# Kernel tuning notes

Measured on AMD Instinct MI355X. Metric: run time of the kernel, lower is better.

The kernel has to match this reference:

```python
import jax, jax.numpy as jnp
import numpy as np
from jax import lax

B, BERT_DIM, Z_DIM, ODE_UNITS, T_MAX = 4096, 768, 64, 128, 512
LN_EPS = 1e-5

def _glorot(key, shape):
    fan_in, fan_out = shape[0], shape[1]
    lim = float(np.sqrt(6.0 / (fan_in + fan_out)))
    return jax.random.uniform(key, shape, jnp.float32, -lim, lim)

def setup_inputs() -> dict:
    key = jax.random.key(0)
    ks = jax.random.split(key, 16)
    inp = {
        'bert_emb': jax.random.normal(ks[0], (B, BERT_DIM), jnp.float32),
        'times': jax.random.uniform(ks[1], (B, T_MAX), jnp.float32),
        'seq_lens': jax.random.randint(ks[2], (B,), 0, T_MAX).astype(jnp.int64),
        'eps': jax.random.normal(ks[3], (B, Z_DIM), jnp.float32),
        # bert_proj: Linear(768->64) + LayerNorm(64)
        'proj_W': _glorot(ks[4], (BERT_DIM, Z_DIM)),
        'proj_b': jnp.zeros((Z_DIM,), jnp.float32),
        'ln_g': jnp.ones((Z_DIM,), jnp.float32),
        'ln_b': jnp.zeros((Z_DIM,), jnp.float32),
        # DiffusionAug
        'log_noise_std': jnp.float32(-2.0),
        'den_W1': _glorot(ks[5], (Z_DIM, 2 * Z_DIM)),
        'den_b1': jnp.zeros((2 * Z_DIM,), jnp.float32),
        'den_W2': _glorot(ks[6], (2 * Z_DIM, Z_DIM)),
        'den_b2': jnp.zeros((Z_DIM,), jnp.float32),
        # ODEFunc: Linear->Tanh->Linear->Tanh->Linear (xavier_uniform, zero bias)
        'ode_W1': _glorot(ks[7], (Z_DIM, ODE_UNITS)),
        'ode_b1': jnp.zeros((ODE_UNITS,), jnp.float32),
        'ode_W2': _glorot(ks[8], (ODE_UNITS, ODE_UNITS)),
        'ode_b2': jnp.zeros((ODE_UNITS,), jnp.float32),
        'ode_W3': _glorot(ks[9], (ODE_UNITS, Z_DIM)),
        'ode_b3': jnp.zeros((Z_DIM,), jnp.float32),
        # dec_head: Linear(64->2)
        'dec_W': _glorot(ks[10], (Z_DIM, 2)),
        'dec_b': jnp.zeros((2,), jnp.float32),
    }
    return inp

def reference(bert_emb, times, seq_lens, eps, proj_W, proj_b, ln_g, ln_b,
              log_noise_std, den_W1, den_b1, den_W2, den_b2,
              ode_W1, ode_b1, ode_W2, ode_b2, ode_W3, ode_b3, dec_W, dec_b):
    T = times.shape[1]
    # bert_proj: Linear + LayerNorm (dropout = identity in eval)
    h = bert_emb @ proj_W + proj_b
    mu = jnp.mean(h, axis=-1, keepdims=True)
    var = jnp.var(h, axis=-1, keepdims=True)
    z_clean = (h - mu) * lax.rsqrt(var + LN_EPS) * ln_g + ln_b
    # DiffusionAug: noise + denoise MLP, MSE to detached clean latent
    sigma = jax.nn.softplus(log_noise_std)
    z_noisy = z_clean + sigma * eps
    z_aug = jax.nn.silu(z_noisy @ den_W1 + den_b1) @ den_W2 + den_b2
    diff_loss = jnp.mean((z_aug - lax.stop_gradient(z_clean)) ** 2)
    # Euler ODE integration: z <- z + dt * f(z), T sequential steps
    dt = jnp.float32(1.0 / max(T, 1))
    def step(z, _):
        f = jnp.tanh(jnp.tanh(z @ ode_W1 + ode_b1) @ ode_W2 + ode_b2) @ ode_W3 + ode_b3
        z_new = z + dt * f
        return z_new, z_new
    _, zs = lax.scan(step, z_aug, None, length=T)  # zs: (T, B, z)
    traj = jnp.concatenate([z_aug[:, None, :], jnp.swapaxes(zs, 0, 1)], axis=1)  # (B, T+1, z)
    out = traj @ dec_W + dec_b  # (B, T+1, 2)
    pred_delta = out[:, :, 0]
    stop_logits = out[:, :, 1]
    return (pred_delta, stop_logits, diff_loss)
```

## Files before the change

### kernel.cpp

```cpp
#include <hip/hip_runtime.h>
#include <stdint.h>

#define NB 4096
#define NT 512
#define OT 513
#define TOTE (NB*OT)
#define LOSSOFF (2*TOTE)

typedef float  f32x4 __attribute__((ext_vector_type(4)));
typedef __fp16 f16x8 __attribute__((ext_vector_type(8)));
typedef __fp16 f16x2 __attribute__((ext_vector_type(2)));

#define MFMA(A,B,C) __builtin_amdgcn_mfma_f32_16x16x32_f16((A),(B),(C),0,0,0)

__device__ __forceinline__ void wg_barrier() {
  asm volatile("s_waitcnt lgkmcnt(0)\n\ts_barrier" ::: "memory");
}

__device__ __forceinline__ float fast_tanh(float x) {
  float e = __builtin_amdgcn_exp2f(x * 2.8853900817779268f);
  return __builtin_fmaf(-2.0f, __builtin_amdgcn_rcpf(1.0f + e), 1.0f);
}
__device__ __forceinline__ float fast_silu(float x) {
  float e = __builtin_amdgcn_exp2f(x * -1.4426950408889634f);
  return x * __builtin_amdgcn_rcpf(1.0f + e);
}
__device__ __forceinline__ uint32_t pk2(float a, float b) {
  union { f16x2 h; uint32_t u; } c;
  c.h = __builtin_amdgcn_cvt_pkrtz(a, b);
  return c.u;
}
__device__ __forceinline__ f16x8 pack8(f32x4 a, f32x4 b) {
  union { f16x8 v; f16x2 h[4]; } u;
  u.h[0] = __builtin_amdgcn_cvt_pkrtz(a.x, a.y);
  u.h[1] = __builtin_amdgcn_cvt_pkrtz(a.z, a.w);
  u.h[2] = __builtin_amdgcn_cvt_pkrtz(b.x, b.y);
  u.h[3] = __builtin_amdgcn_cvt_pkrtz(b.z, b.w);
  return u.v;
}

#define WS_CBUF (256u<<10)

__global__ void prep_kernel(const float* __restrict__ oW1, const float* __restrict__ oW2,
                            const float* __restrict__ dW,  const float* __restrict__ dW1,
                            const float* __restrict__ dW2, const float* __restrict__ pW,
                            const float* __restrict__ oW3, const float* __restrict__ ob3,
                            char* __restrict__ wdst, float* __restrict__ cbuf,
                            float* __restrict__ dout) {
  const float dtc = 1.0f / 512.0f;
  if (blockIdx.x == 57) {
    int tid = threadIdx.x;
    if (tid < 144) {
      float s = 0.f;
      if (tid < 128) {
        for (int k = 0; k < 64; k++) s = __builtin_fmaf(ob3[k], oW1[k * 128 + tid], s);
      } else if (tid < 130) {
        int cc = tid - 128;
        for (int k = 0; k < 64; k++) s = __builtin_fmaf(ob3[k], dW[k * 2 + cc], s);
      }
      cbuf[tid] = s * dtc;
    }
    if (tid == 255) dout[LOSSOFF] = 0.0f;
    return;
  }
  int g = blockIdx.x * 256 + threadIdx.x;
  int fid = g >> 6, lane = g & 63;
  if (fid >= 50 && fid < 64) return;
  int m4 = lane & 15;
  int k0 = (lane >> 4) * 8;
  if (fid >= 48 && fid < 50) {
    int kt = fid - 48;
    int kb = kt * 32 + k0;
    f16x8 out;
    #pragma unroll
    for (int j = 0; j < 8; j++) out[j] = (m4 < 2) ? (__fp16)dW[(kb + j) * 2 + m4] : (__fp16)0.f;
    *(f16x8*)(wdst + (size_t)(fid * 64 + lane) * 16) = out;
    return;
  }
  if (fid >= 192) {
    int local = fid - 192;
    int mt = local >> 2, kt = local & 3;
    int m  = mt * 16 + m4;
    int kb = kt * 32 + k0;
    f16x8 out;
    #pragma unroll
    for (int j = 0; j < 8; j++) {
      int k = kb + j;
      float s = 0.f;
      if (m < 128) {
        #pragma unroll 4
        for (int i = 0; i < 64; i++) s = __builtin_fmaf(oW3[k * 64 + i], oW1[i * 128 + m], s);
      } else if (m < 130) {
        for (int i = 0; i < 64; i++) s = __builtin_fmaf(oW3[k * 64 + i], dW[i * 2 + (m - 128)], s);
      }
      out[j] = (__fp16)(s * dtc);
    }
    *(f16x8*)(wdst + (size_t)(fid * 64 + lane) * 16) = out;
    return;
  }
  const float* src; int Kt, M, base;
  if      (fid < 16)  { src = oW1;  Kt = 2;  M = 128; base = 0;  }
  else if (fid < 48)  { src = oW2;  Kt = 4;  M = 128; base = 16; }
  else if (fid < 80)  { src = dW1;  Kt = 2;  M = 128; base = 64; }
  else if (fid < 96)  { src = dW2;  Kt = 4;  M = 64;  base = 80; }
  else                { src = pW;   Kt = 24; M = 64;  base = 96; }
  int local = fid - base;
  int mt = local / Kt, kt = local % Kt;
  int m  = mt * 16 + m4;
  int kb = kt * 32 + k0;
  f16x8 out;
  #pragma unroll
  for (int j = 0; j < 8; j++) out[j] = (__fp16)src[(size_t)(kb + j) * M + m];
  *(f16x8*)(wdst + (size_t)(fid * 64 + lane) * 16) = out;
}

__global__ __launch_bounds__(512, 1) void main_kernel(
    const float* __restrict__ bert, const float* __restrict__ eps,
    const float* __restrict__ projb, const float* __restrict__ lng,
    const float* __restrict__ lnb,  const float* __restrict__ lns,
    const float* __restrict__ db1,  const float* __restrict__ db2,
    const float* __restrict__ ob1,  const float* __restrict__ ob2,
    const float* __restrict__ decb, const char* __restrict__ wpack,
    const float* __restrict__ cbuf, float* __restrict__ dout) {
  __shared__ __attribute__((aligned(16))) char sZ[16 * 128];
  __shared__ __attribute__((aligned(16))) char sH[16 * 256];
  __shared__ f32x4  sScr[4 * 64];
  __shared__ float2 sMV[64];
  __shared__ float  sLsum[4];
  __shared__ __attribute__((aligned(16))) char sH1[4096];
  __shared__ __attribute__((aligned(16))) char sH2[4096];

  const int tid  = threadIdx.x;
  const int wave = tid >> 6, lane = tid & 63;
  const int q = lane >> 4, b = lane & 15;
  const int bg = blockIdx.x * 16 + b;
  const int b7 = b & 7;
  const f16x8* wp = (const f16x8*)wpack;
  const int u0 = wave * 16 + q * 4;
  const f32x4 zero4 = {0,0,0,0};

  const int zr0 = b * 128 + ((q    ) ^ b7) * 16;
  const int zr1 = b * 128 + ((q + 4) ^ b7) * 16;
  int hr[4];
  #pragma unroll
  for (int s = 0; s < 4; s++) hr[s] = b * 256 + ((4 * s + q) ^ b7) * 16;
  const int hw = b * 256 + (((2 * wave + (q >> 1)) ^ b7) * 16) + (q & 1) * 8;
  const int zw = b * 128 + (((2 * (wave & 3) + (q >> 1)) ^ b7) * 16) + (q & 1) * 8;

  {
    const int mt = wave & 3, kh = wave >> 2;
    f32x4 hA = {0,0,0,0}, hB = {0,0,0,0};
    #pragma unroll 4
    for (int i = 0; i < 12; i++) {
      int kt = kh * 12 + i;
      f16x8 af = wp[(size_t)(96 + mt * 24 + kt) * 64 + lane];
      const float* bp = bert + (size_t)bg * 768 + kt * 32 + q * 8;
      f32x4 f0 = *(const f32x4*)bp;
      f32x4 f1 = *(const f32x4*)(bp + 4);
      f16x8 bf = pack8(f0, f1);
      if (i & 1) hB = MFMA(af, bf, hB); else hA = MFMA(af, bf, hA);
    }
    f32x4 hacc = hA + hB;
    if (wave >= 4) sScr[(wave - 4) * 64 + lane] = hacc;
    __syncthreads();

    f32x4 h = {0,0,0,0}, zc = {0,0,0,0};
    if (wave < 4) {
      h = hacc + sScr[wave * 64 + lane];
      h.x += projb[u0 + 0]; h.y += projb[u0 + 1];
      h.z += projb[u0 + 2]; h.w += projb[u0 + 3];
      float s1 = h.x + h.y + h.z + h.w;
      float s2 = h.x*h.x + h.y*h.y + h.z*h.z + h.w*h.w;
      s1 += __shfl_xor(s1, 16); s1 += __shfl_xor(s1, 32);
      s2 += __shfl_xor(s2, 16); s2 += __shfl_xor(s2, 32);
      if (q == 0) sMV[wave * 16 + b] = make_float2(s1, s2);
    }
    __syncthreads();
    if (wave < 4) {
      float t1 = 0.f, t2 = 0.f;
      #pragma unroll
      for (int w2 = 0; w2 < 4; w2++) { float2 m = sMV[w2 * 16 + b]; t1 += m.x; t2 += m.y; }
      float mu  = t1 * (1.0f / 64.0f);
      float var = t2 * (1.0f / 64.0f) - mu * mu;
      float rs  = rsqrtf(var + 1e-5f);
      float sigma = logf(1.0f + expf(lns[0]));
      f32x4 e = *(const f32x4*)(eps + (size_t)bg * 64 + u0);
      zc.x = __builtin_fmaf((h.x - mu) * rs, lng[u0+0], lnb[u0+0]);
      zc.y = __builtin_fmaf((h.y - mu) * rs, lng[u0+1], lnb[u0+1]);
      zc.z = __builtin_fmaf((h.z - mu) * rs, lng[u0+2], lnb[u0+2]);
      zc.w = __builtin_fmaf((h.w - mu) * rs, lng[u0+3], lnb[u0+3]);
      f32x4 zn = zc + sigma * e;
      *(uint2*)(sZ + zw) = make_uint2(pk2(zn.x, zn.y), pk2(zn.z, zn.w));
    }
    __syncthreads();
    {
      f16x8 w0 = wp[(size_t)(64 + wave * 2 + 0) * 64 + lane];
      f16x8 w1 = wp[(size_t)(64 + wave * 2 + 1) * 64 + lane];
      f16x8 bz0 = *(const f16x8*)(sZ + zr0);
      f16x8 bz1 = *(const f16x8*)(sZ + zr1);
      f32x4 bias = { db1[u0+0], db1[u0+1], db1[u0+2], db1[u0+3] };
      f32x4 acc = MFMA(w0, bz0, bias);
      acc = MFMA(w1, bz1, acc);
      *(uint2*)(sH + hw) = make_uint2(pk2(fast_silu(acc.x), fast_silu(acc.y)),
                                      pk2(fast_silu(acc.z), fast_silu(acc.w)));
    }
    __syncthreads();
    if (wave < 4) {
      f16x8 w0 = wp[(size_t)(80 + wave * 4 + 0) * 64 + lane];
      f16x8 w1 = wp[(size_t)(80 + wave * 4 + 1) * 64 + lane];
      f16x8 w2 = wp[(size_t)(80 + wave * 4 + 2) * 64 + lane];
      f16x8 w3 = wp[(size_t)(80 + wave * 4 + 3) * 64 + lane];
      f16x8 g0 = *(const f16x8*)(sH + hr[0]);
      f16x8 g1 = *(const f16x8*)(sH + hr[1]);
      f16x8 g2 = *(const f16x8*)(sH + hr[2]);
      f16x8 g3 = *(const f16x8*)(sH + hr[3]);
      f32x4 bias = { db2[u0+0], db2[u0+1], db2[u0+2], db2[u0+3] };
      f32x4 aA = MFMA(w0, g0, bias); aA = MFMA(w1, g1, aA);
      f32x4 aB = MFMA(w2, g2, zero4); aB = MFMA(w3, g3, aB);
      f32x4 za = aA + aB;
      *(uint2*)(sZ + zw) = make_uint2(pk2(za.x, za.y), pk2(za.z, za.w));
      f32x4 d = za - zc;
      float sl = d.x*d.x + d.y*d.y + d.z*d.z + d.w*d.w;
      const int offs[6] = {1, 2, 4, 8, 16, 32};
      #pragma unroll
      for (int i = 0; i < 6; i++) sl += __shfl_xor(sl, offs[i]);
      if (lane == 0) sLsum[wave] = sl;
    }
    __syncthreads();
    if (tid == 0)
      atomicAdd(dout + LOSSOFF,
                (sLsum[0] + sLsum[1] + sLsum[2] + sLsum[3]) * (1.0f / 262144.0f));
  }

  int rd[4];
  #pragma unroll
  for (int kt = 0; kt < 4; kt++) rd[kt] = b * 256 + (((kt * 4 + q) ^ b) * 16);
  const int wr = b * 256 + (((wave * 2 + (q >> 1)) ^ b) * 16) + (q & 1) * 8;

  f16x8 w2f[4], uf[4], uf8[4];
  #pragma unroll
  for (int kt = 0; kt < 4; kt++) {
    w2f[kt] = wp[(size_t)(16  + wave * 4 + kt) * 64 + lane];
    uf [kt] = wp[(size_t)(192 + wave * 4 + kt) * 64 + lane];
  }
  if (wave == 7) {
    #pragma unroll
    for (int kt = 0; kt < 4; kt++)
      uf8[kt] = wp[(size_t)(192 + 32 + kt) * 64 + lane];
  }
  const f32x4 b2f = *(const f32x4*)(ob2  + wave * 16 + q * 4);
  const f32x4 cw  = *(const f32x4*)(cbuf + wave * 16 + q * 4);
  const f32x4 c8  = *(const f32x4*)(cbuf + 128 + q * 4);

  f16x8 zf0 = *(const f16x8*)(sZ + zr0);
  f16x8 zf1 = *(const f16x8*)(sZ + zr1);
  f32x4 b1v = *(const f32x4*)(ob1 + wave * 16 + q * 4);
  f32x4 G = MFMA(wp[(size_t)(wave * 2 + 0) * 64 + lane], zf0, b1v);
  G = MFMA(wp[(size_t)(wave * 2 + 1) * 64 + lane], zf1, G);
  *(uint2*)(sH1 + wr) = make_uint2(pk2(fast_tanh(G.x), fast_tanh(G.y)),
                                   pk2(fast_tanh(G.z), fast_tanh(G.w)));

  f32x4 Gd = zero4;
  float* const outp_p = dout + (size_t)bg * OT;
  float* const outp_s = dout + (size_t)TOTE + (size_t)bg * OT;
  if (wave == 7) {
    f32x4 b1d = zero4;
    if (q == 0) { b1d.x = decb[0]; b1d.y = decb[1]; }
    Gd = MFMA(wp[(size_t)48 * 64 + lane], zf0, b1d);
    Gd = MFMA(wp[(size_t)49 * 64 + lane], zf1, Gd);
    if (q == 0) { outp_p[0] = Gd.x; outp_s[0] = Gd.y; }
  }
  wg_barrier();

  #pragma unroll 1
  for (int t = 0; t < NT; ++t) {
    f16x8 p0 = *(const f16x8*)(sH1 + rd[0]);
    f16x8 p1 = *(const f16x8*)(sH1 + rd[1]);
    f16x8 p2 = *(const f16x8*)(sH1 + rd[2]);
    f16x8 p3 = *(const f16x8*)(sH1 + rd[3]);
    f32x4 a  = MFMA(w2f[0], p0, b2f);
    a  = MFMA(w2f[1], p1, a);
    f32x4 a2 = MFMA(w2f[2], p2, zero4);
    a2 = MFMA(w2f[3], p3, a2);
    f32x4 hv = a + a2;
    *(uint2*)(sH2 + wr) = make_uint2(pk2(fast_tanh(hv.x), fast_tanh(hv.y)),
                                     pk2(fast_tanh(hv.z), fast_tanh(hv.w)));
    wg_barrier();

    f16x8 g0 = *(const f16x8*)(sH2 + rd[0]);
    f16x8 g1 = *(const f16x8*)(sH2 + rd[1]);
    f16x8 g2 = *(const f16x8*)(sH2 + rd[2]);
    f16x8 g3 = *(const f16x8*)(sH2 + rd[3]);
    f32x4 d  = MFMA(uf[0], g0, G);
    d  = MFMA(uf[1], g1, d);
    f32x4 d2 = MFMA(uf[2], g2, cw);
    d2 = MFMA(uf[3], g3, d2);
    G = d + d2;
    *(uint2*)(sH1 + wr) = make_uint2(pk2(fast_tanh(G.x), fast_tanh(G.y)),
                                     pk2(fast_tanh(G.z), fast_tanh(G.w)));
    if (wave == 7) {
      f32x4 e  = MFMA(uf8[0], g0, Gd);
      e  = MFMA(uf8[1], g1, e);
      f32x4 e2 = MFMA(uf8[2], g2, c8);
      e2 = MFMA(uf8[3], g3, e2);
      Gd = e + e2;
      if (q == 0) { outp_p[t + 1] = Gd.x; outp_s[t + 1] = Gd.y; }
    }
    wg_barrier();
  }
}

extern "C" void kernel_launch(void* const* d_in, const int* in_sizes, int n_in,
                              void* d_out, int out_size, void* d_ws, size_t ws_size,
                              hipStream_t stream) {
  const float* bert  = (const float*)d_in[0];
  const float* eps   = (const float*)d_in[3];
  const float* projW = (const float*)d_in[4];
  const float* projb = (const float*)d_in[5];
  const float* lng   = (const float*)d_in[6];
  const float* lnb   = (const float*)d_in[7];
  const float* lns   = (const float*)d_in[8];
  const float* denW1 = (const float*)d_in[9];
  const float* denb1 = (const float*)d_in[10];
  const float* denW2 = (const float*)d_in[11];
  const float* denb2 = (const float*)d_in[12];
  const float* odeW1 = (const float*)d_in[13];
  const float* odeb1 = (const float*)d_in[14];
  const float* odeW2 = (const float*)d_in[15];
  const float* odeb2 = (const float*)d_in[16];
  const float* odeW3 = (const float*)d_in[17];
  const float* odeb3 = (const float*)d_in[18];
  const float* decW  = (const float*)d_in[19];
  const float* decb  = (const float*)d_in[20];
  float* dout = (float*)d_out;

  char*  wpak = (char*)d_ws;
  float* cbuf = (float*)((char*)d_ws + WS_CBUF);

  prep_kernel<<<58, 256, 0, stream>>>(odeW1, odeW2, decW, denW1, denW2, projW,
                                      odeW3, odeb3, wpak, cbuf, dout);
  main_kernel<<<256, 512, 0, stream>>>(bert, eps, projb, lng, lnb, lns,
                                       denb1, denb2, odeb1, odeb2, decb,
                                       wpak, cbuf, dout);
}
```

Baseline: 435.0 us.

## Fold weight packing prep kernel into main kernel and unroll time loop by two

Measured after the change: 523.0 us. +20.2%, slower.

```diff
diff --git a/kernel.cpp b/kernel.cpp
--- a/kernel.cpp
+++ b/kernel.cpp
@@ -39,79 +39,37 @@
   return u.v;
 }
 
-#define WS_CBUF (256u<<10)
-
-__global__ void prep_kernel(const float* __restrict__ oW1, const float* __restrict__ oW2,
-                            const float* __restrict__ dW,  const float* __restrict__ dW1,
-                            const float* __restrict__ dW2, const float* __restrict__ pW,
-                            const float* __restrict__ oW3, const float* __restrict__ ob3,
-                            char* __restrict__ wdst, float* __restrict__ cbuf,
-                            float* __restrict__ dout) {
+__device__ __forceinline__ f16x8 gather_frag(const float* __restrict__ src,
+                                             int M, int m, int kb) {
+  f16x8 out;
+  #pragma unroll
+  for (int j = 0; j < 8; j++) out[j] = (__fp16)src[(size_t)(kb + j) * M + m];
+  return out;
+}
+
+__device__ __forceinline__ f16x8 compute_ufrag(const float* __restrict__ oW3,
+                                               const float* __restrict__ oW1,
+                                               const float* __restrict__ dW,
+                                               int m, int kb) {
   const float dtc = 1.0f / 512.0f;
-  if (blockIdx.x == 57) {
-    int tid = threadIdx.x;
-    if (tid < 144) {
-      float s = 0.f;
-      if (tid < 128) {
-        for (int k = 0; k < 64; k++) s = __builtin_fmaf(ob3[k], oW1[k * 128 + tid], s);
-      } else if (tid < 130) {
-        int cc = tid - 128;
-        for (int k = 0; k < 64; k++) s = __builtin_fmaf(ob3[k], dW[k * 2 + cc], s);
-      }
-      cbuf[tid] = s * dtc;
-    }
-    if (tid == 255) dout[LOSSOFF] = 0.0f;
-    return;
-  }
-  int g = blockIdx.x * 256 + threadIdx.x;
-  int fid = g >> 6, lane = g & 63;
-  if (fid >= 50 && fid < 64) return;
-  int m4 = lane & 15;
-  int k0 = (lane >> 4) * 8;
-  if (fid >= 48 && fid < 50) {
-    int kt = fid - 48;
-    int kb = kt * 32 + k0;
-    f16x8 out;
-    #pragma unroll
-    for (int j = 0; j < 8; j++) out[j] = (m4 < 2) ? (__fp16)dW[(kb + j) * 2 + m4] : (__fp16)0.f;
-    *(f16x8*)(wdst + (size_t)(fid * 64 + lane) * 16) = out;
-    return;
-  }
-  if (fid >= 192) {
-    int local = fid - 192;
-    int mt = local >> 2, kt = local & 3;
-    int m  = mt * 16 + m4;
-    int kb = kt * 32 + k0;
-    f16x8 out;
-    #pragma unroll
-    for (int j = 0; j < 8; j++) {
-      int k = kb + j;
-      float s = 0.f;
-      if (m < 128) {
-        #pragma unroll 4
-        for (int i = 0; i < 64; i++) s = __builtin_fmaf(oW3[k * 64 + i], oW1[i * 128 + m], s);
-      } else if (m < 130) {
-        for (int i = 0; i < 64; i++) s = __builtin_fmaf(oW3[k * 64 + i], dW[i * 2 + (m - 128)], s);
-      }
-      out[j] = (__fp16)(s * dtc);
-    }
-    *(f16x8*)(wdst + (size_t)(fid * 64 + lane) * 16) = out;
-    return;
-  }
-  const float* src; int Kt, M, base;
-  if      (fid < 16)  { src = oW1;  Kt = 2;  M = 128; base = 0;  }
-  else if (fid < 48)  { src = oW2;  Kt = 4;  M = 128; base = 16; }
-  else if (fid < 80)  { src = dW1;  Kt = 2;  M = 128; base = 64; }
-  else if (fid < 96)  { src = dW2;  Kt = 4;  M = 64;  base = 80; }
-  else                { src = pW;   Kt = 24; M = 64;  base = 96; }
-  int local = fid - base;
-  int mt = local / Kt, kt = local % Kt;
-  int m  = mt * 16 + m4;
-  int kb = kt * 32 + k0;
   f16x8 out;
   #pragma unroll
-  for (int j = 0; j < 8; j++) out[j] = (__fp16)src[(size_t)(kb + j) * M + m];
-  *(f16x8*)(wdst + (size_t)(fid * 64 + lane) * 16) = out;
+  for (int j = 0; j < 8; j++) {
+    int k = kb + j;
+    float s = 0.f;
+    if (m < 128) {
+      #pragma unroll 4
+      for (int i = 0; i < 64; i++) s = __builtin_fmaf(oW3[k * 64 + i], oW1[i * 128 + m], s);
+    } else if (m < 130) {
+      for (int i = 0; i < 64; i++) s = __builtin_fmaf(oW3[k * 64 + i], dW[i * 2 + (m - 128)], s);
+    }
+    out[j] = (__fp16)(s * dtc);
+  }
+  return out;
+}
+
+__global__ void zero_loss_kernel(float* __restrict__ dout) {
+  if (threadIdx.x == 0) dout[LOSSOFF] = 0.0f;
 }
 
 __global__ __launch_bounds__(512, 1) void main_kernel(
@@ -120,8 +78,12 @@
     const float* __restrict__ lnb,  const float* __restrict__ lns,
     const float* __restrict__ db1,  const float* __restrict__ db2,
     const float* __restrict__ ob1,  const float* __restrict__ ob2,
-    const float* __restrict__ decb, const char* __restrict__ wpack,
-    const float* __restrict__ cbuf, float* __restrict__ dout) {
+    const float* __restrict__ decb,
+    const float* __restrict__ oW1,  const float* __restrict__ oW2,
+    const float* __restrict__ oW3,  const float* __restrict__ ob3,
+    const float* __restrict__ dW,   const float* __restrict__ dW1,
+    const float* __restrict__ dW2,  const float* __restrict__ pW,
+    float* __restrict__ dout) {
   __shared__ __attribute__((aligned(16))) char sZ[16 * 128];
   __shared__ __attribute__((aligned(16))) char sH[16 * 256];
   __shared__ f32x4  sScr[4 * 64];
@@ -135,9 +97,10 @@
   const int q = lane >> 4, b = lane & 15;
   const int bg = blockIdx.x * 16 + b;
   const int b7 = b & 7;
-  const f16x8* wp = (const f16x8*)wpack;
   const int u0 = wave * 16 + q * 4;
+  const int q8 = q * 8;
   const f32x4 zero4 = {0,0,0,0};
+  const float dtc = 1.0f / 512.0f;
 
   const int zr0 = b * 128 + ((q    ) ^ b7) * 16;
   const int zr1 = b * 128 + ((q + 4) ^ b7) * 16;
@@ -153,8 +116,8 @@
     #pragma unroll 4
     for (int i = 0; i < 12; i++) {
       int kt = kh * 12 + i;
-      f16x8 af = wp[(size_t)(96 + mt * 24 + kt) * 64 + lane];
-      const float* bp = bert + (size_t)bg * 768 + kt * 32 + q * 8;
+      f16x8 af = gather_frag(pW, 64, mt * 16 + b, kt * 32 + q8);
+      const float* bp = bert + (size_t)bg * 768 + kt * 32 + q8;
       f32x4 f0 = *(const f32x4*)bp;
       f32x4 f1 = *(const f32x4*)(bp + 4);
       f16x8 bf = pack8(f0, f1);
@@ -194,8 +157,8 @@
     }
     __syncthreads();
     {
-      f16x8 w0 = wp[(size_t)(64 + wave * 2 + 0) * 64 + lane];
-      f16x8 w1 = wp[(size_t)(64 + wave * 2 + 1) * 64 + lane];
+      f16x8 w0 = gather_frag(dW1, 128, wave * 16 + b, 0 * 32 + q8);
+      f16x8 w1 = gather_frag(dW1, 128, wave * 16 + b, 1 * 32 + q8);
       f16x8 bz0 = *(const f16x8*)(sZ + zr0);
       f16x8 bz1 = *(const f16x8*)(sZ + zr1);
       f32x4 bias = { db1[u0+0], db1[u0+1], db1[u0+2], db1[u0+3] };
@@ -206,10 +169,10 @@
     }
     __syncthreads();
     if (wave < 4) {
-      f16x8 w0 = wp[(size_t)(80 + wave * 4 + 0) * 64 + lane];
-      f16x8 w1 = wp[(size_t)(80 + wave * 4 + 1) * 64 + lane];
-      f16x8 w2 = wp[(size_t)(80 + wave * 4 + 2) * 64 + lane];
-      f16x8 w3 = wp[(size_t)(80 + wave * 4 + 3) * 64 + lane];
+      f16x8 w0 = gather_frag(dW2, 64, wave * 16 + b, 0 * 32 + q8);
+      f16x8 w1 = gather_frag(dW2, 64, wave * 16 + b, 1 * 32 + q8);
+      f16x8 w2 = gather_frag(dW2, 64, wave * 16 + b, 2 * 32 + q8);
+      f16x8 w3 = gather_frag(dW2, 64, wave * 16 + b, 3 * 32 + q8);
       f16x8 g0 = *(const f16x8*)(sH + hr[0]);
       f16x8 g1 = *(const f16x8*)(sH + hr[1]);
       f16x8 g2 = *(const f16x8*)(sH + hr[2]);
@@ -240,23 +203,33 @@
   f16x8 w2f[4], uf[4], uf8[4];
   #pragma unroll
   for (int kt = 0; kt < 4; kt++) {
-    w2f[kt] = wp[(size_t)(16  + wave * 4 + kt) * 64 + lane];
-    uf [kt] = wp[(size_t)(192 + wave * 4 + kt) * 64 + lane];
+    w2f[kt] = gather_frag(oW2, 128, wave * 16 + b, kt * 32 + q8);
+    uf [kt] = compute_ufrag(oW3, oW1, dW, wave * 16 + b, kt * 32 + q8);
   }
   if (wave == 7) {
     #pragma unroll
     for (int kt = 0; kt < 4; kt++)
-      uf8[kt] = wp[(size_t)(192 + 32 + kt) * 64 + lane];
-  }
-  const f32x4 b2f = *(const f32x4*)(ob2  + wave * 16 + q * 4);
-  const f32x4 cw  = *(const f32x4*)(cbuf + wave * 16 + q * 4);
-  const f32x4 c8  = *(const f32x4*)(cbuf + 128 + q * 4);
+      uf8[kt] = compute_ufrag(oW3, oW1, dW, 128 + b, kt * 32 + q8);
+  }
+  const f32x4 b2f = *(const f32x4*)(ob2 + wave * 16 + q * 4);
+  f32x4 cw, c8;
+  #pragma unroll
+  for (int r = 0; r < 4; r++) {
+    int u = wave * 16 + q * 4 + r;
+    float s = 0.f;
+    for (int k = 0; k < 64; k++) s = __builtin_fmaf(ob3[k], oW1[k * 128 + u], s);
+    cw[r] = s * dtc;
+    int m = 128 + q * 4 + r;
+    float s8 = 0.f;
+    if (m < 130) for (int k = 0; k < 64; k++) s8 = __builtin_fmaf(ob3[k], dW[k * 2 + (m - 128)], s8);
+    c8[r] = s8 * dtc;
+  }
 
   f16x8 zf0 = *(const f16x8*)(sZ + zr0);
   f16x8 zf1 = *(const f16x8*)(sZ + zr1);
   f32x4 b1v = *(const f32x4*)(ob1 + wave * 16 + q * 4);
-  f32x4 G = MFMA(wp[(size_t)(wave * 2 + 0) * 64 + lane], zf0, b1v);
-  G = MFMA(wp[(size_t)(wave * 2 + 1) * 64 + lane], zf1, G);
+  f32x4 G = MFMA(gather_frag(oW1, 128, wave * 16 + b, 0 * 32 + q8), zf0, b1v);
+  G = MFMA(gather_frag(oW1, 128, wave * 16 + b, 1 * 32 + q8), zf1, G);
   *(uint2*)(sH1 + wr) = make_uint2(pk2(fast_tanh(G.x), fast_tanh(G.y)),
                                    pk2(fast_tanh(G.z), fast_tanh(G.w)));
 
@@ -264,15 +237,21 @@
   float* const outp_p = dout + (size_t)bg * OT;
   float* const outp_s = dout + (size_t)TOTE + (size_t)bg * OT;
   if (wave == 7) {
+    f16x8 d0, d1;
+    #pragma unroll
+    for (int j = 0; j < 8; j++) {
+      d0[j] = (b < 2) ? (__fp16)dW[(0 * 32 + q8 + j) * 2 + b] : (__fp16)0.f;
+      d1[j] = (b < 2) ? (__fp16)dW[(1 * 32 + q8 + j) * 2 + b] : (__fp16)0.f;
+    }
     f32x4 b1d = zero4;
     if (q == 0) { b1d.x = decb[0]; b1d.y = decb[1]; }
-    Gd = MFMA(wp[(size_t)48 * 64 + lane], zf0, b1d);
-    Gd = MFMA(wp[(size_t)49 * 64 + lane], zf1, Gd);
+    Gd = MFMA(d0, zf0, b1d);
+    Gd = MFMA(d1, zf1, Gd);
     if (q == 0) { outp_p[0] = Gd.x; outp_s[0] = Gd.y; }
   }
   wg_barrier();
 
-  #pragma unroll 1
+  #pragma unroll 2
   for (int t = 0; t < NT; ++t) {
     f16x8 p0 = *(const f16x8*)(sH1 + rd[0]);
     f16x8 p1 = *(const f16x8*)(sH1 + rd[1]);
@@ -334,12 +313,9 @@
   const float* decb  = (const float*)d_in[20];
   float* dout = (float*)d_out;
 
-  char*  wpak = (char*)d_ws;
-  float* cbuf = (float*)((char*)d_ws + WS_CBUF);
-
-  prep_kernel<<<58, 256, 0, stream>>>(odeW1, odeW2, decW, denW1, denW2, projW,
-                                      odeW3, odeb3, wpak, cbuf, dout);
+  zero_loss_kernel<<<1, 64, 0, stream>>>(dout);
   main_kernel<<<256, 512, 0, stream>>>(bert, eps, projb, lng, lnb, lns,
                                        denb1, denb2, odeb1, odeb2, decb,
-                                       wpak, cbuf, dout);
-}
+                                       odeW1, odeW2, odeW3, odeb3,
+                                       decW, denW1, denW2, projW, dout);
+}
```
